# Kernel optimization log

Hardware: AMD Instinct MI355X
Metric: run time of the kernel (lower is better)

The kernel has to match this reference:

```python
import jax, jax.numpy as jnp
import numpy as np

B, T, HID = 2, 2048, 1024
H, DK, DV = 8, 128, 128      # num_heads, head_f_dim (key), head_i_dim (value)
LR = 128                     # gate low-rank dim
EPS = 1e-5


def setup_inputs() -> dict:
    key = jax.random.key(0)
    ks = jax.random.split(key, 8)
    def w(k, shape, fan_in):
        return jax.random.normal(k, shape, jnp.float32) / np.float32(np.sqrt(fan_in))
    return {
        "hidden_states": jax.random.normal(ks[0], (B, T, HID), jnp.float32),
        "Wq": w(ks[1], (HID, HID), HID),   # key_dim x hidden
        "Wk": w(ks[2], (HID, HID), HID),
        "Wv": w(ks[3], (HID, HID), HID),   # value_dim x hidden
        "Wg1": w(ks[4], (LR, HID), HID),   # low-rank gate down
        "Wg2": w(ks[5], (HID, LR), LR),    # low-rank gate up
        "g_norm_weight": jnp.ones((HID,), jnp.float32),
        "Wo": w(ks[6], (HID, HID), HID),
    }


def _lightnet_fwd(x, Wq, Wk, Wv, Wg1, Wg2, g_norm_weight, Wo):
    b, t, _ = x.shape
    q = jax.nn.silu(x @ Wq.T).reshape(b, t, H, DK)
    k = (x @ Wk.T).reshape(b, t, H, DK)
    v = (x @ Wv.T).reshape(b, t, H, DV)

    # LightNet gating: normalized keys via logcumsumexp over time
    z = jax.lax.cumlogsumexp(k, axis=1)                 # [b,t,h,dk]
    k = jnp.exp(k - z)                                  # exp-normalized keys
    g = jnp.concatenate([z[:, :1], z[:, :-1]], axis=1) - z  # <= 0; g[:,0]=0

    scale = DK ** -0.5

    # gated linear attention recurrence: S_t = exp(g_t) * S_{t-1} + k_t v_t^T
    def step(S, inp):
        qt, kt, vt, gt = inp                            # [b,h,dk],[b,h,dk],[b,h,dv],[b,h,dk]
        S = jnp.exp(gt)[..., None] * S + kt[..., None] * vt[..., None, :]
        o = jnp.einsum('bhk,bhkv->bhv', qt, S) * scale
        return S, o

    S0 = jnp.zeros((b, H, DK, DV), x.dtype)
    tfirst = lambda a: jnp.moveaxis(a, 1, 0)
    _, oT = jax.lax.scan(step, S0, (tfirst(q), tfirst(k), tfirst(v), tfirst(g)))
    o = jnp.moveaxis(oT, 0, 1).reshape(b, t, H * DV)    # [b,t,hidden]

    # RMSNorm(o) * swish(gate) then output projection
    gate = (x @ Wg1.T) @ Wg2.T
    o = o * jax.lax.rsqrt(jnp.mean(o * o, axis=-1, keepdims=True) + EPS) * g_norm_weight
    o = o * gate * jax.nn.sigmoid(gate)
    return o @ Wo.T


def reference(hidden_states, Wq, Wk, Wv, Wg1, Wg2, g_norm_weight, Wo):
    return _lightnet_fwd(hidden_states, Wq, Wk, Wv, Wg1, Wg2, g_norm_weight, Wo)
```

## Files before the change

### kernel.cpp

```cpp
#include <hip/hip_runtime.h>
#include <hip/hip_bf16.h>
#include <stdint.h>


typedef short short8 __attribute__((ext_vector_type(8)));
typedef float f32x4 __attribute__((ext_vector_type(4)));

#define T_SEQ 2048
#define HIDN  1024
#define SCALE 0.08838834764831845f
#define LDSP  136

__device__ __forceinline__ float blo(unsigned int u){
  union{unsigned int i; float f;} v; v.i = u << 16; return v.f;
}
__device__ __forceinline__ float bhi(unsigned int u){
  union{unsigned int i; float f;} v; v.i = u & 0xffff0000u; return v.f;
}
__device__ __forceinline__ float bu2f(unsigned short u){
  union{unsigned int i; float f;} v; v.i = ((unsigned int)u) << 16; return v.f;
}
__device__ __forceinline__ unsigned short f2bu(float f){
  union{float f; unsigned int i;} v; v.f = f;
  unsigned int x = v.i;
  x += 0x7fffu + ((x >> 16) & 1u);
  return (unsigned short)(x >> 16);
}
__device__ __forceinline__ void up8(const unsigned short* p, float* f){
  uint4 v = *(const uint4*)p;
  f[0]=blo(v.x); f[1]=bhi(v.x); f[2]=blo(v.y); f[3]=bhi(v.y);
  f[4]=blo(v.z); f[5]=bhi(v.z); f[6]=blo(v.w); f[7]=bhi(v.w);
}
__device__ __forceinline__ void async16(const void* g, void* l){
  __builtin_amdgcn_global_load_lds(
      (const __attribute__((address_space(1))) unsigned int*)g,
      (__attribute__((address_space(3))) unsigned int*)l, 16, 0, 0);
}

__global__ __launch_bounds__(256) void convert_all(
    const float* __restrict__ X,  const float* __restrict__ Wq,
    const float* __restrict__ Wk, const float* __restrict__ Wv,
    const float* __restrict__ Wg1,const float* __restrict__ Wg2,
    const float* __restrict__ gnw,const float* __restrict__ Wo,
    unsigned short* __restrict__ base, float* __restrict__ SumSq)
{
  int q = blockIdx.x * 256 + threadIdx.x;
  const float* src; unsigned short* dst; int rel = q;
  if (rel < 1048576)            { src = X;   dst = base;            }
  else if ((rel -= 1048576) < 262144) { src = Wq;  dst = base + 4194304; }
  else if ((rel -=  262144) < 262144) { src = Wk;  dst = base + 5242880; }
  else if ((rel -=  262144) < 262144) { src = Wv;  dst = base + 6291456; }
  else if ((rel -=  262144) < 262144) { src = Wo;  dst = base + 7340032; }
  else if ((rel -=  262144) <  32768) { src = Wg1; dst = base + 8388608; }
  else if ((rel -=   32768) <  32768) { src = Wg2; dst = base + 8519680; }
  else if ((rel -=   32768) <    256) { src = gnw; dst = base + 8650752; }
  else { rel -= 256;
    ((float4*)SumSq)[rel] = make_float4(0.f,0.f,0.f,0.f); return; }
  float4 v = ((const float4*)src)[rel];
  ushort4 o; o.x=f2bu(v.x); o.y=f2bu(v.y); o.z=f2bu(v.z); o.w=f2bu(v.w);
  ((ushort4*)dst)[rel] = o;
}

__device__ __forceinline__ void gemm_core(
    const unsigned short* __restrict__ A, const unsigned short* __restrict__ B,
    int K, int row0, int col0,
    unsigned short* sA, unsigned short* sB, f32x4 acc[4][4], int tid)
{
  const int lane = tid & 63;
  const int wm = (tid >> 6) & 1, wn = tid >> 7;
  const int wb = tid & 192;
  for (int k0 = 0; k0 < K; k0 += 64){
    __syncthreads();
#pragma unroll
    for (int h = 0; h < 2; ++h){
#pragma unroll
      for (int r = 0; r < 2; ++r){
        int idx  = r*256 + tid;
        int mrow = idx >> 2, kc = (idx & 3) * 8;
        async16(A + (size_t)(row0 + mrow)*K + k0 + h*32 + kc,
                sA + (size_t)(h*512 + r*256 + wb)*8);
        async16(B + (size_t)(col0 + mrow)*K + k0 + h*32 + kc,
                sB + (size_t)(h*512 + r*256 + wb)*8);
      }
    }
    __syncthreads();
#pragma unroll
    for (int h = 0; h < 2; ++h){
      short8 av[4], bv[4];
#pragma unroll
      for (int i=0;i<4;i++)
        av[i] = *(const short8*)(sA + h*4096 + (size_t)(wm*64 + i*16 + (lane&15))*32 + (lane>>4)*8);
#pragma unroll
      for (int j=0;j<4;j++)
        bv[j] = *(const short8*)(sB + h*4096 + (size_t)(wn*64 + j*16 + (lane&15))*32 + (lane>>4)*8);
#pragma unroll
      for (int i=0;i<4;i++)
#pragma unroll
        for (int j=0;j<4;j++)
          acc[i][j] = __builtin_amdgcn_mfma_f32_16x16x32_bf16(av[i], bv[j], acc[i][j], 0, 0, 0);
    }
  }
}

__device__ __forceinline__ void epilogue_lds(
    f32x4 acc[4][4], int row0, int col0, int tid, int ldc, int act,
    unsigned short* __restrict__ Cb, unsigned short* sC)
{
  const int lane = tid & 63;
  const int wm = (tid >> 6) & 1, wn = tid >> 7;
#pragma unroll
  for (int p=0;p<4;p++){
    __syncthreads();
    if (wm == (p>>1)){
#pragma unroll
      for (int ii=0; ii<2; ii++){
        int i = (p&1)*2 + ii;
        int lr = i*16 + ((lane>>4)<<2) - (p&1)*32;
#pragma unroll
        for (int j=0;j<4;j++){
          int col = wn*64 + j*16 + (lane&15);
#pragma unroll
          for (int r=0;r<4;r++){
            float v = acc[i][j][r];
            if (act == 1) v = v / (1.f + __expf(-v));
            else if (act == 2) v = __expf(v);
            sC[(lr+r)*128 + col] = f2bu(v);
          }
        }
      }
    }
    __syncthreads();
#pragma unroll
    for (int c = tid; c < 512; c += 256){
      int rr = c >> 4, off = (c & 15)*8;
      *(uint4*)&Cb[(size_t)(row0 + p*32 + rr)*ldc + col0 + off] =
          *(const uint4*)&sC[rr*128 + off];
    }
  }
}

__device__ __forceinline__ void epilogue_f32(
    f32x4 acc[4][4], int row0, int col0, int tid, int ldc,
    float* __restrict__ Cf)
{
  const int lane = tid & 63;
  const int wm = (tid >> 6) & 1, wn = tid >> 7;
#pragma unroll
  for (int i=0;i<4;i++){
    int rbase = row0 + wm*64 + i*16 + ((lane>>4)<<2);
#pragma unroll
    for (int j=0;j<4;j++){
      int col = col0 + wn*64 + j*16 + (lane&15);
#pragma unroll
      for (int r=0;r<4;r++)
        Cf[(size_t)(rbase + r)*ldc + col] = acc[i][j][r];
    }
  }
}

__global__ __launch_bounds__(256, 4) void proj_kernel(
    const unsigned short* __restrict__ X,
    const unsigned short* __restrict__ Wq, const unsigned short* __restrict__ Wk,
    const unsigned short* __restrict__ Wv, const unsigned short* __restrict__ Wg1,
    unsigned short* __restrict__ Qb, unsigned short* __restrict__ Eb,
    unsigned short* __restrict__ Vb, unsigned short* __restrict__ G1b)
{
  __shared__ unsigned short sA[128*64], sB[128*64];
  int tid = threadIdx.x;
  int which = blockIdx.y >> 3;
  const unsigned short* Bp = (which==0)?Wq:(which==1)?Wk:(which==2)?Wv:Wg1;
  int row0 = blockIdx.x * 128;
  int col0 = (which==3) ? 0 : (blockIdx.y & 7) * 128;
  f32x4 acc[4][4] = {};
  gemm_core(X, Bp, HIDN, row0, col0, sA, sB, acc, tid);
  if      (which==0) epilogue_lds(acc,row0,col0,tid,HIDN,1,Qb, sA);
  else if (which==1) epilogue_lds(acc,row0,col0,tid,HIDN,2,Eb, sA);
  else if (which==2) epilogue_lds(acc,row0,col0,tid,HIDN,0,Vb, sA);
  else               epilogue_lds(acc,row0,col0,tid,128 ,0,G1b,sA);
}

__global__ __launch_bounds__(256, 4) void gemm_bt(
    const unsigned short* __restrict__ A, const unsigned short* __restrict__ B,
    int K, int ldc, int act, float* __restrict__ Cf,
    unsigned short* __restrict__ Cb)
{
  __shared__ unsigned short sA[128*64], sB[128*64];
  int tid = threadIdx.x;
  int row0 = blockIdx.x * 128, col0 = blockIdx.y * 128;
  f32x4 acc[4][4] = {};
  gemm_core(A, B, K, row0, col0, sA, sB, acc, tid);
  if (Cb) epilogue_lds(acc, row0, col0, tid, ldc, act, Cb, sA);
  else    epilogue_f32(acc, row0, col0, tid, ldc, Cf);
}

__global__ __launch_bounds__(512, 2) void attn_pass1(
    const unsigned short* __restrict__ Eb, const unsigned short* __restrict__ Vb,
    unsigned short* __restrict__ U, float* __restrict__ Esum)
{
  __shared__ unsigned short Vt[128*LDSP], Et[128*LDSP];
  __shared__ float seg_part[4*128];
  int tid = threadIdx.x;
  const int lane = tid & 63, quad = lane >> 4;
  const int w = tid >> 6, wm = w & 3, wn = w >> 2;
  const int Rb = wm*32, Cb = wn*64;
  int bh = blockIdx.x >> 4, ch = blockIdx.x & 15;
  int b = bh >> 3, h = bh & 7;
  size_t rowbase = (size_t)(b*T_SEQ + ch*128)*HIDN + h*128;

#pragma unroll
  for (int i=0;i<4;i++){
    int u = tid + i*512; int t = u >> 4, kc = (u & 15)*8;
    unsigned short tmp[8];
    *(uint4*)tmp = *(const uint4*)&Vb[rowbase + (size_t)t*HIDN + kc];
#pragma unroll
    for (int j=0;j<8;j++) Vt[(kc+j)*LDSP + t] = tmp[j];
    *(uint4*)tmp = *(const uint4*)&Eb[rowbase + (size_t)t*HIDN + kc];
#pragma unroll
    for (int j=0;j<8;j++) Et[(kc+j)*LDSP + t] = tmp[j];
  }
  __syncthreads();

  {
    int seg = tid >> 7, k = tid & 127;
    float s = 0.f;
    for (int c = seg*32; c < seg*32+32; ++c) s += bu2f(Et[k*LDSP + c]);
    seg_part[seg*128 + k] = s;
  }
  __syncthreads();
  if (tid < 128)
    Esum[(size_t)blockIdx.x*128 + tid] =
        seg_part[tid] + seg_part[128+tid] + seg_part[256+tid] + seg_part[384+tid];

  f32x4 acc[2][4] = {};
  short8 av[2], bv[4];
#pragma unroll
  for (int s0=0; s0<128; s0+=32){
#pragma unroll
    for (int i=0;i<2;i++)
      av[i] = *(const short8*)(Vt + (Rb + i*16 + (lane&15))*LDSP + s0 + quad*8);
#pragma unroll
    for (int j=0;j<4;j++)
      bv[j] = *(const short8*)(Et + (Cb + j*16 + (lane&15))*LDSP + s0 + quad*8);
#pragma unroll
    for (int i=0;i<2;i++)
#pragma unroll
      for (int j=0;j<4;j++)
        acc[i][j] = __builtin_amdgcn_mfma_f32_16x16x32_bf16(av[i], bv[j], acc[i][j], 0,0,0);
  }
  __syncthreads();

#pragma unroll
  for (int i=0;i<2;i++)
#pragma unroll
    for (int j=0;j<4;j++){
      int k = Cb + j*16 + (lane&15);
#pragma unroll
      for (int r=0;r<4;r++){
        int v = Rb + i*16 + quad*4 + r;
        Et[v*LDSP + k] = f2bu(acc[i][j][r]);
      }
    }
  __syncthreads();
  unsigned short* Ub = U + (size_t)blockIdx.x*16384;
#pragma unroll
  for (int i=0;i<4;i++){
    int u = tid + i*512; int v = u >> 4, kc = (u & 15)*8;
    *(uint4*)&Ub[v*128 + kc] = *(const uint4*)&Et[v*LDSP + kc];
  }
}

__global__ __launch_bounds__(256) void attn_pass2(
    unsigned short* __restrict__ U, float* __restrict__ Esum)
{
  int bh = blockIdx.x >> 4, sl = blockIdx.x & 15;
  int p = sl*1024 + threadIdx.x*4;
  float r0=0.f, r1=0.f, r2=0.f, r3=0.f;
  for (int c=0;c<16;c++){
    ushort4* ptr = (ushort4*)&U[(size_t)(bh*16 + c)*16384 + p];
    ushort4 t = *ptr;
    ushort4 w;
    w.x=f2bu(r0); w.y=f2bu(r1); w.z=f2bu(r2); w.w=f2bu(r3);
    *ptr = w;
    r0 += bu2f(t.x); r1 += bu2f(t.y); r2 += bu2f(t.z); r3 += bu2f(t.w);
  }
  if (sl == 0 && threadIdx.x < 128){
    float r = 0.f;
    for (int c=0;c<16;c++){
      float* q = &Esum[(size_t)(bh*16 + c)*128 + threadIdx.x];
      float t = *q; *q = r; r += t;
    }
  }
}

__global__ __launch_bounds__(512, 4) void attn_pass3(
    const unsigned short* __restrict__ Eb, const unsigned short* __restrict__ Qb,
    const unsigned short* __restrict__ Vb, const unsigned short* __restrict__ U,
    const float* __restrict__ Esum, unsigned short* __restrict__ Oatt,
    float* __restrict__ SumSq)
{
  __shared__ unsigned short smem[2*128*LDSP];
  __shared__ float seg_part[4*128];
  unsigned short* bufA = smem;
  unsigned short* bufB = smem + 128*LDSP;

  int tid = threadIdx.x;
  const int lane = tid & 63, quad = lane >> 4;
  const int w = tid >> 6, wm = w & 3, wn = w >> 2;
  const int Rb = wm*32, Cb = wn*64;
  int bh = blockIdx.x >> 4, ch = blockIdx.x & 15;
  int b = bh >> 3, h = bh & 7;
  size_t rowbase = (size_t)(b*T_SEQ + ch*128)*HIDN + h*128;
  const unsigned short* Ublk = U + (size_t)blockIdx.x*16384;

#pragma unroll
  for (int i=0;i<4;i++){
    int u = tid + i*512; int t = u >> 4, kc = (u & 15)*8;
    *(uint4*)&bufA[t*LDSP + kc] = *(const uint4*)&Qb[rowbase + (size_t)t*HIDN + kc];
    *(uint4*)&bufB[t*LDSP + kc] = *(const uint4*)&Eb[rowbase + (size_t)t*HIDN + kc];
  }
  __syncthreads();

  {
    int col = tid & 127, seg = tid >> 7;
    float psum = 0.f;
    for (int s = seg*32; s < seg*32+32; ++s) psum += bu2f(bufB[s*LDSP + col]);
    seg_part[seg*128 + col] = psum;
    __syncthreads();
    float run = Esum[(size_t)blockIdx.x*128 + col];
    for (int ss=0; ss<4; ++ss) if (ss < seg) run += seg_part[ss*128 + col];
    for (int s = seg*32; s < seg*32+32; ++s){
      run += bu2f(bufB[s*LDSP + col]);
      float q = bu2f(bufA[s*LDSP + col]);
      bufA[s*LDSP + col] = f2bu(q * SCALE * __builtin_amdgcn_rcpf(run));
    }
  }
  __syncthreads();

  f32x4 accO[2][4] = {}, accP[2][4] = {};
  short8 av[2], bv[4];
#pragma unroll
  for (int k0=0; k0<128; k0+=32){
#pragma unroll
    for (int i=0;i<2;i++)
      av[i] = *(const short8*)(bufA + (Rb + i*16 + (lane&15))*LDSP + k0 + quad*8);
#pragma unroll
    for (int j=0;j<4;j++)
      bv[j] = *(const short8*)(Ublk + (size_t)(Cb + j*16 + (lane&15))*128 + k0 + quad*8);
#pragma unroll
    for (int i=0;i<2;i++)
#pragma unroll
      for (int j=0;j<4;j++)
        accO[i][j] = __builtin_amdgcn_mfma_f32_16x16x32_bf16(av[i], bv[j], accO[i][j], 0,0,0);
#pragma unroll
    for (int j=0;j<4;j++)
      bv[j] = *(const short8*)(bufB + (Cb + j*16 + (lane&15))*LDSP + k0 + quad*8);
#pragma unroll
    for (int i=0;i<2;i++)
#pragma unroll
      for (int j=0;j<4;j++)
        accP[i][j] = __builtin_amdgcn_mfma_f32_16x16x32_bf16(av[i], bv[j], accP[i][j], 0,0,0);
  }
  __syncthreads();

#pragma unroll
  for (int i=0;i<2;i++){
#pragma unroll
    for (int j=0;j<4;j++){
      int s = Cb + j*16 + (lane&15);
#pragma unroll
      for (int r=0;r<4;r++){
        int t = Rb + i*16 + quad*4 + r;
        bufA[t*LDSP + s] = f2bu(s <= t ? accP[i][j][r] : 0.f);
      }
    }
  }
#pragma unroll
  for (int i=0;i<4;i++){
    int u = tid + i*512; int t = u >> 4, kc = (u & 15)*8;
    unsigned short tmp[8];
    *(uint4*)tmp = *(const uint4*)&Vb[rowbase + (size_t)t*HIDN + kc];
#pragma unroll
    for (int j=0;j<8;j++) bufB[(kc+j)*LDSP + t] = tmp[j];
  }
  __syncthreads();

#pragma unroll
  for (int k0=0; k0<128; k0+=32){
#pragma unroll
    for (int i=0;i<2;i++)
      av[i] = *(const short8*)(bufA + (Rb + i*16 + (lane&15))*LDSP + k0 + quad*8);
#pragma unroll
    for (int j=0;j<4;j++)
      bv[j] = *(const short8*)(bufB + (Cb + j*16 + (lane&15))*LDSP + k0 + quad*8);
#pragma unroll
    for (int i=0;i<2;i++)
#pragma unroll
      for (int j=0;j<4;j++)
        accO[i][j] = __builtin_amdgcn_mfma_f32_16x16x32_bf16(av[i], bv[j], accO[i][j], 0,0,0);
  }
  __syncthreads();

#pragma unroll
  for (int i=0;i<2;i++){
#pragma unroll
    for (int j=0;j<4;j++){
      int v = Cb + j*16 + (lane&15);
#pragma unroll
      for (int r=0;r<4;r++){
        int t = Rb + i*16 + quad*4 + r;
        bufA[t*LDSP + v] = f2bu(accO[i][j][r]);
      }
    }
  }
  __syncthreads();

  {
    int seg = tid >> 7, row = tid & 127;
    float s = 0.f;
    for (int c = seg*32; c < seg*32+32; ++c){
      float x = bu2f(bufA[row*LDSP + c]); s += x*x;
    }
    seg_part[seg*128 + row] = s;
  }
#pragma unroll
  for (int i=0;i<4;i++){
    int u = tid + i*512; int t = u >> 4, kc = (u & 15)*8;
    *(uint4*)&Oatt[rowbase + (size_t)t*HIDN + kc] = *(const uint4*)&bufA[t*LDSP + kc];
  }
  __syncthreads();
  if (tid < 128){
    float s = seg_part[tid] + seg_part[128+tid] + seg_part[256+tid] + seg_part[384+tid];
    atomicAdd(&SumSq[(size_t)b*T_SEQ + ch*128 + tid], s);
  }
}

__global__ __launch_bounds__(256) void norm_gate2(
    const unsigned short* __restrict__ Oatt, const unsigned short* __restrict__ Gt,
    const unsigned short* __restrict__ gnw, const float* __restrict__ SumSq,
    unsigned short* __restrict__ Onorm)
{
  int row = blockIdx.x, tid = threadIdx.x;
  float rstd = rsqrtf(SumSq[row] * (1.f/1024.f) + 1e-5f);
  ushort4 o4 = *(const ushort4*)&Oatt[(size_t)row*HIDN + tid*4];
  ushort4 g4 = *(const ushort4*)&Gt  [(size_t)row*HIDN + tid*4];
  ushort4 w4 = *(const ushort4*)&gnw[tid*4];
  ushort4 r4;
  r4.x = f2bu(bu2f(o4.x) * rstd * bu2f(w4.x) * bu2f(g4.x));
  r4.y = f2bu(bu2f(o4.y) * rstd * bu2f(w4.y) * bu2f(g4.y));
  r4.z = f2bu(bu2f(o4.z) * rstd * bu2f(w4.z) * bu2f(g4.z));
  r4.w = f2bu(bu2f(o4.w) * rstd * bu2f(w4.w) * bu2f(g4.w));
  *(ushort4*)&Onorm[(size_t)row*HIDN + tid*4] = r4;
}

extern "C" void kernel_launch(void* const* d_in, const int* in_sizes, int n_in,
                              void* d_out, int out_size, void* d_ws, size_t ws_size,
                              hipStream_t stream) {
  unsigned short* wsS = (unsigned short*)d_ws;

  unsigned short* Xc   = wsS;
  unsigned short* Wqc  = wsS + 4194304;
  unsigned short* Wkc  = wsS + 5242880;
  unsigned short* Wvc  = wsS + 6291456;
  unsigned short* Woc  = wsS + 7340032;
  unsigned short* Wg1c = wsS + 8388608;
  unsigned short* Wg2c = wsS + 8519680;
  unsigned short* gnwc = wsS + 8650752;
  unsigned short* Qb   = wsS + 8651776;
  unsigned short* Eb   = wsS + 12846080;
  unsigned short* Vb   = wsS + 17040384;
  unsigned short* G1b  = wsS + 21234688;
  unsigned short* Gt   = wsS + 21758976;
  unsigned short* Ub   = wsS + 25953280;
  unsigned short* Oattb= wsS + 30147584;
  float*          Esum = (float*)(wsS + 34341888);
  float*          SumSq= (float*)(wsS + 34407424);
  unsigned short* Onorm = Qb;

  convert_all<<<8453, 256, 0, stream>>>(
      (const float*)d_in[0], (const float*)d_in[1], (const float*)d_in[2],
      (const float*)d_in[3], (const float*)d_in[4], (const float*)d_in[5],
      (const float*)d_in[6], (const float*)d_in[7], wsS, SumSq);

  proj_kernel<<<dim3(32,25), 256, 0, stream>>>(Xc, Wqc, Wkc, Wvc, Wg1c, Qb, Eb, Vb, G1b);
  gemm_bt   <<<dim3(32,8),  256, 0, stream>>>(G1b, Wg2c, 128, HIDN, 1, nullptr, Gt);
  attn_pass1<<<256, 512, 0, stream>>>(Eb, Vb, Ub, Esum);
  attn_pass2<<<256, 256, 0, stream>>>(Ub, Esum);
  attn_pass3<<<256, 512, 0, stream>>>(Eb, Qb, Vb, Ub, Esum, Oattb, SumSq);
  norm_gate2<<<4096, 256, 0, stream>>>(Oattb, Gt, gnwc, SumSq, Onorm);
  gemm_bt   <<<dim3(32,8),  256, 0, stream>>>(Onorm, Woc, HIDN, HIDN, 0,
                                              (float*)d_out, nullptr);
}
```

Measured before the change: 207.0 us.

## Replace projection GEMM with 256x256-tile pipelined fused QKV kernel

Swaps the 128x128-tile projection kernel for a 512-thread kernel using 256x256 output tiles, treating Wq/Wk/Wv as one contiguous weight matrix. It adds double-buffered async global-to-LDS loads with XOR-swizzled layout, explicit vmcnt waits and hard barriers that interleave loads with MFMA phases. The aim is more data reuse per block and better overlap of memory with compute. In exchange the grid is only 208 blocks, which may underfill the device. The hand-tuned wait counts are fragile.

```diff
diff --git a/kernel.cpp b/kernel.cpp
--- a/kernel.cpp
+++ b/kernel.cpp
@@ -36,6 +36,14 @@
       (const __attribute__((address_space(1))) unsigned int*)g,
       (__attribute__((address_space(3))) unsigned int*)l, 16, 0, 0);
 }
+__device__ __forceinline__ void hard_barrier(){
+  __builtin_amdgcn_sched_barrier(0);
+  asm volatile("" ::: "memory");
+  __builtin_amdgcn_s_barrier();
+  asm volatile("" ::: "memory");
+  __builtin_amdgcn_sched_barrier(0);
+}
+#define VMWAIT(N) asm volatile("s_waitcnt vmcnt(" #N ")" ::: "memory")
 
 __global__ __launch_bounds__(256) void convert_all(
     const float* __restrict__ X,  const float* __restrict__ Wq,
@@ -61,6 +69,145 @@
   ((ushort4*)dst)[rel] = o;
 }
 
+__global__ __launch_bounds__(512, 2) void proj256(
+    const unsigned short* __restrict__ X,
+    const unsigned short* __restrict__ Wqkv,
+    const unsigned short* __restrict__ Wg1,
+    unsigned short* __restrict__ QEV,
+    unsigned short* __restrict__ G1b)
+{
+  __shared__ unsigned short smem[65536];
+  const int tid  = threadIdx.x;
+  const int lane = tid & 63;
+  const int w    = tid >> 6;
+  const int wm   = w >> 2, wn = w & 3;
+  const int q    = lane >> 4, l15 = lane & 15;
+  const int brow = blockIdx.x * 256;
+  const bool isG1 = (blockIdx.y == 12);
+  const unsigned short* Bp = isG1 ? Wg1 : Wqkv;
+  const int bcol = isG1 ? 0 : blockIdx.y * 256;
+
+  f32x4 acc[2][2][4][2] = {};
+  short8 bA[8], bB0[4], bB1[4];
+
+  auto STAGE = [&](int tt, int mat, int hf){
+    const unsigned short* src = mat ? Bp + (size_t)(bcol + hf*128)*1024
+                                    : X  + (size_t)(brow + hf*128)*1024;
+    unsigned short* dst = smem + (((tt&1)*2 + mat)*2 + hf)*8192;
+    const int k0 = tt*64;
+#pragma unroll
+    for (int r=0;r<2;r++){
+      int cb = r*512 + w*64;
+      int c  = cb + lane;
+      int rh = c >> 3;
+      int colS = ((c & 7)*8) ^ ((rh & 7) << 3);
+      async16(src + (size_t)rh*1024 + k0 + colS, dst + cb*8);
+    }
+  };
+  auto LDA = [&](int MQ, int buf){
+#pragma unroll
+    for (int i=0;i<4;i++){
+      int rh = wm*64 + i*16 + l15;
+      const unsigned short* base = smem + ((buf*2 + 0)*2 + MQ)*8192 + rh*64;
+#pragma unroll
+      for (int kk=0;kk<2;kk++)
+        bA[i*2+kk] = *(const short8*)(base + (((kk*32) + q*8) ^ ((rh&7)<<3)));
+    }
+  };
+  auto LDB = [&](short8 (&bB)[4], int NQ, int buf){
+#pragma unroll
+    for (int j=0;j<2;j++){
+      int rh = wn*32 + j*16 + l15;
+      const unsigned short* base = smem + ((buf*2 + 1)*2 + NQ)*8192 + rh*64;
+#pragma unroll
+      for (int kk=0;kk<2;kk++)
+        bB[j*2+kk] = *(const short8*)(base + (((kk*32) + q*8) ^ ((rh&7)<<3)));
+    }
+  };
+  auto MMA = [&](f32x4 (&AC)[4][2], short8 (&BV)[4]){
+    __builtin_amdgcn_s_setprio(1);
+#pragma unroll
+    for (int i=0;i<4;i++)
+#pragma unroll
+      for (int j=0;j<2;j++)
+#pragma unroll
+        for (int kk=0;kk<2;kk++)
+          AC[i][j] = __builtin_amdgcn_mfma_f32_16x16x32_bf16(
+              bA[i*2+kk], BV[j*2+kk], AC[i][j], 0, 0, 0);
+    __builtin_amdgcn_s_setprio(0);
+  };
+
+  STAGE(0,0,0); STAGE(0,1,0); STAGE(0,0,1); STAGE(0,1,1);
+  STAGE(1,0,0); STAGE(1,1,0); STAGE(1,0,1);
+  VMWAIT(6);
+  hard_barrier();
+
+#pragma unroll 2
+  for (int u=0; u<16; ++u){
+    const int buf = u & 1;
+    LDA(0, buf); LDB(bB0, 0, buf);
+    if (u < 15) STAGE(u+1, 1, 1);
+    hard_barrier();
+    MMA(acc[0][0], bB0);
+    if (u < 15) { VMWAIT(8); } else { VMWAIT(0); }
+    hard_barrier();
+    LDB(bB1, 1, buf);
+    if (u < 14) STAGE(u+2, 0, 0);
+    hard_barrier();
+    MMA(acc[0][1], bB1);
+    hard_barrier();
+    LDA(1, buf);
+    if (u < 14) STAGE(u+2, 1, 0);
+    hard_barrier();
+    MMA(acc[1][0], bB0);
+    hard_barrier();
+    if (u < 14) STAGE(u+2, 0, 1);
+    hard_barrier();
+    MMA(acc[1][1], bB1);
+    if (u < 14) { VMWAIT(10); } else { VMWAIT(4); }
+    hard_barrier();
+  }
+
+  unsigned short* sC = smem;
+#pragma unroll
+  for (int MQ=0;MQ<2;MQ++)
+#pragma unroll
+    for (int NQ=0;NQ<2;NQ++){
+      const int m = isG1 ? 3 : ((blockIdx.y*256 + NQ*128) >> 10);
+#pragma unroll
+      for (int i=0;i<4;i++)
+#pragma unroll
+        for (int j=0;j<2;j++)
+#pragma unroll
+          for (int r=0;r<4;r++){
+            float v = acc[MQ][NQ][i][j][r];
+            if (m == 0) v = v / (1.f + __expf(-v));
+            else if (m == 1) v = __expf(v);
+            int rr = wm*64 + i*16 + q*4 + r;
+            int cc = wn*32 + j*16 + l15;
+            sC[rr*132 + cc] = f2bu(v);
+          }
+      __syncthreads();
+      if (!(isG1 && NQ == 1)){
+#pragma unroll
+        for (int k=0;k<4;k++){
+          int c = tid + k*512;
+          int row = c >> 4, col8 = (c & 15)*8;
+          int gr = brow + MQ*128 + row;
+          uint4 val = *(const uint4*)(sC + row*132 + col8);
+          if (isG1)
+            *(uint4*)(G1b + (size_t)gr*128 + col8) = val;
+          else {
+            int gcol = blockIdx.y*256 + NQ*128 + col8;
+            *(uint4*)(QEV + (size_t)(gcol>>10)*4194304
+                          + (size_t)gr*1024 + (gcol & 1023)) = val;
+          }
+        }
+      }
+      __syncthreads();
+    }
+}
+
 __device__ __forceinline__ void gemm_core(
     const unsigned short* __restrict__ A, const unsigned short* __restrict__ B,
     int K, int row0, int col0,
@@ -156,27 +303,6 @@
         Cf[(size_t)(rbase + r)*ldc + col] = acc[i][j][r];
     }
   }
-}
-
-__global__ __launch_bounds__(256, 4) void proj_kernel(
-    const unsigned short* __restrict__ X,
-    const unsigned short* __restrict__ Wq, const unsigned short* __restrict__ Wk,
-    const unsigned short* __restrict__ Wv, const unsigned short* __restrict__ Wg1,
-    unsigned short* __restrict__ Qb, unsigned short* __restrict__ Eb,
-    unsigned short* __restrict__ Vb, unsigned short* __restrict__ G1b)
-{
-  __shared__ unsigned short sA[128*64], sB[128*64];
-  int tid = threadIdx.x;
-  int which = blockIdx.y >> 3;
-  const unsigned short* Bp = (which==0)?Wq:(which==1)?Wk:(which==2)?Wv:Wg1;
-  int row0 = blockIdx.x * 128;
-  int col0 = (which==3) ? 0 : (blockIdx.y & 7) * 128;
-  f32x4 acc[4][4] = {};
-  gemm_core(X, Bp, HIDN, row0, col0, sA, sB, acc, tid);
-  if      (which==0) epilogue_lds(acc,row0,col0,tid,HIDN,1,Qb, sA);
-  else if (which==1) epilogue_lds(acc,row0,col0,tid,HIDN,2,Eb, sA);
-  else if (which==2) epilogue_lds(acc,row0,col0,tid,HIDN,0,Vb, sA);
-  else               epilogue_lds(acc,row0,col0,tid,128 ,0,G1b,sA);
 }
 
 __global__ __launch_bounds__(256, 4) void gemm_bt(
@@ -459,12 +585,10 @@
 
   unsigned short* Xc   = wsS;
   unsigned short* Wqc  = wsS + 4194304;
-  unsigned short* Wkc  = wsS + 5242880;
-  unsigned short* Wvc  = wsS + 6291456;
-  unsigned short* Woc  = wsS + 7340032;
   unsigned short* Wg1c = wsS + 8388608;
   unsigned short* Wg2c = wsS + 8519680;
   unsigned short* gnwc = wsS + 8650752;
+  unsigned short* Woc  = wsS + 7340032;
   unsigned short* Qb   = wsS + 8651776;
   unsigned short* Eb   = wsS + 12846080;
   unsigned short* Vb   = wsS + 17040384;
@@ -481,7 +605,7 @@
       (const float*)d_in[3], (const float*)d_in[4], (const float*)d_in[5],
       (const float*)d_in[6], (const float*)d_in[7], wsS, SumSq);
 
-  proj_kernel<<<dim3(32,25), 256, 0, stream>>>(Xc, Wqc, Wkc, Wvc, Wg1c, Qb, Eb, Vb, G1b);
+  proj256   <<<dim3(16,13), 512, 0, stream>>>(Xc, Wqc, Wg1c, Qb, G1b);
   gemm_bt   <<<dim3(32,8),  256, 0, stream>>>(G1b, Wg2c, 128, HIDN, 1, nullptr, Gt);
   attn_pass1<<<256, 512, 0, stream>>>(Eb, Vb, Ub, Esum);
   attn_pass2<<<256, 256, 0, stream>>>(Ub, Esum);
```

Result: slower. 238.4 us (+15.1%).
